# Kernel tuning notes

Hardware: AMD Instinct MI355X
Metric: run time of the kernel (lower is better)

The kernel has to match this reference:

```python
import jax, jax.numpy as jnp
import numpy as np

MARGIN = 0.3
BIG = 9999999.0


def setup_inputs() -> dict:
    key = jax.random.key(0)
    k1, k2, k3 = jax.random.split(key, 3)
    N, D, D2, NUM_IDS = 8192, 1024, 512, 512
    emb = jax.random.normal(k1, (N, D), dtype=jnp.float32)
    clot_feats_s = jax.random.normal(k2, (N, D2), dtype=jnp.float32)
    label = jax.random.randint(k3, (N,), 0, NUM_IDS, dtype=jnp.int64)
    return {"emb": emb, "label": label, "clot_feats_s": clot_feats_s}


def _margin_ranking_loss(x1, x2, y, margin):
    # torch MarginRankingLoss: mean(max(0, -y*(x1-x2)+margin))
    return jnp.mean(jnp.maximum(0.0, -y * (x1 - x2) + margin))


def reference(emb, label, clot_feats_s):
    N = emb.shape[0]
    # euclidean_dist(emb, emb): [N,N]
    sq = jnp.sum(emb * emb, axis=1)
    dist = sq[:, None] + sq[None, :] - 2.0 * (emb @ emb.T)
    dist = jnp.sqrt(jnp.clip(dist, 1e-12, None))
    # cosine similarity of clot_feats_s with itself: [N,N]
    nrm = jnp.sqrt(jnp.sum(clot_feats_s * clot_feats_s, axis=1))
    cos = (clot_feats_s @ clot_feats_s.T) / (nrm[:, None] * nrm[None, :])
    # same-identity mask
    sim = (label[:, None] == label[None, :]).astype(dist.dtype)
    # batch-hard: top-2 positives (largest masked distance), hardest negative (smallest)
    pos_vals, pos_idx = jax.lax.top_k(dist - BIG * (1.0 - sim), 2)
    dist_ap1, dist_ap2 = pos_vals[:, 0], pos_vals[:, 1]
    neg_mat = dist + BIG * sim
    hard_n_idx = jnp.argmin(neg_mat, axis=1)
    dist_an = jnp.min(neg_mat, axis=1)
    rows = jnp.arange(N)
    # per-row gathers into cosine-sim matrix (detached in original)
    alpha1 = jax.lax.stop_gradient(cos[rows, pos_idx[:, 0]])
    alpha2 = jax.lax.stop_gradient(cos[rows, pos_idx[:, 1]])
    # (alphan gathered in original but unused in the loss)
    y11 = jnp.where(alpha1 < alpha2, -1.0, 1.0)
    y11_m = jnp.where(alpha1 == alpha2, 0.0, 1.0)
    loss11 = _margin_ranking_loss(
        dist_ap2 * y11_m,
        dist_ap1 * y11_m + MARGIN * (alpha1 - alpha2 - y11),
        y11, MARGIN)
    dist_ap1_m = dist_ap1 + MARGIN * (alpha1 - 1.0)
    loss13 = _margin_ranking_loss(dist_an, dist_ap1_m, 1.0, MARGIN)
    loss = 0.1 * loss11 + loss13
    prec = jnp.mean((dist_an > dist_ap1_m).astype(jnp.float32))
    return loss, prec
```

## Files before the change

### kernel.cpp

```cpp
#include <hip/hip_runtime.h>
#include <stdint.h>

#define NR 8192
#define DE 1024
#define DC 512
#define BIGF 9999999.0f
#define MARG 0.3f
#define NEGI -3.0e38f
#define POSI 3.0e38f

typedef __attribute__((ext_vector_type(8))) short bf16x8;
typedef __attribute__((ext_vector_type(4))) float f32x4;

typedef __attribute__((address_space(3))) unsigned int lds_u32;
typedef const __attribute__((address_space(1))) unsigned int glb_u32;

static __device__ __forceinline__ void ld_g2l16(const void* g, void* l) {
    __builtin_amdgcn_global_load_lds((glb_u32*)g, (lds_u32*)l, 16, 0, 0);
}

static __device__ __forceinline__ unsigned short f2bf(float x) {
    unsigned u = __float_as_uint(x);
    unsigned r = u + 0x7FFFu + ((u >> 16) & 1u);
    return (unsigned short)(r >> 16);
}

static __device__ __forceinline__ float b2f(short u) {
    return __uint_as_float(((unsigned)(unsigned short)u) << 16);
}

__global__ __launch_bounds__(256) void k_prep_emb(const float* __restrict__ emb,
                                                  const int* __restrict__ label,
                                                  short* __restrict__ embb,
                                                  float* __restrict__ sq,
                                                  int* __restrict__ cnt) {
    int row = blockIdx.x, tid = threadIdx.x;
    float4 v = ((const float4*)(emb + (size_t)row * DE))[tid];
    float s = v.x * v.x + v.y * v.y + v.z * v.z + v.w * v.w;
    ushort4 b;
    b.x = f2bf(v.x); b.y = f2bf(v.y); b.z = f2bf(v.z); b.w = f2bf(v.w);
    *(ushort4*)&embb[(size_t)row * DE + tid * 4] = b;
    for (int m = 1; m < 64; m <<= 1) s += __shfl_xor(s, m);
    __shared__ float red[4];
    if ((tid & 63) == 0) red[tid >> 6] = s;
    __syncthreads();
    if (tid == 0) {
        sq[row] = red[0] + red[1] + red[2] + red[3];
        atomicAdd(&cnt[label[row]], 1);
    }
}

__global__ __launch_bounds__(256) void k_fill(const int* __restrict__ cnt,
                                              const int* __restrict__ label,
                                              int* __restrict__ clsOff,
                                              int* __restrict__ fill,
                                              int* __restrict__ list) {
    __shared__ int s[512];
    int t = threadIdx.x;
    s[t] = cnt[t];
    s[t + 256] = cnt[t + 256];
    __syncthreads();
    for (int d = 1; d < 512; d <<= 1) {
        int v0 = (t >= d) ? s[t - d] : 0;
        int v1 = s[t + 256 - d];
        __syncthreads();
        s[t] += v0;
        s[t + 256] += v1;
        __syncthreads();
    }
    if (blockIdx.x == 0) {
        clsOff[t] = s[t] - cnt[t];
        clsOff[t + 256] = s[t + 256] - cnt[t + 256];
    }
    int i = blockIdx.x * 256 + t;
    int l = label[i];
    int p = atomicAdd(&fill[l], 1);
    list[s[l] - cnt[l] + p] = i;
}

__global__ __launch_bounds__(256, 4) void k_main(const short* __restrict__ embb,
                                                 const float* __restrict__ sq,
                                                 const int* __restrict__ label,
                                                 unsigned* __restrict__ mnA) {
    const int b = blockIdx.x;
    int r = (int)((129.0f - sqrtf(16641.0f - 8.0f * (float)b)) * 0.5f);
    if (r < 0) r = 0;
    if (r > 63) r = 63;
    while (r > 0 && 64 * r - (r * (r - 1)) / 2 > b) --r;
    while (64 * (r + 1) - ((r + 1) * r) / 2 <= b) ++r;
    const int c = r + (b - (64 * r - (r * (r - 1)) / 2));
    const int i0 = r * 128, j0 = c * 128;

    __shared__ __align__(16) short As[128 * 32];
    __shared__ __align__(16) short Bs[128 * 32];

    const int tid = threadIdx.x;
    const int lane = tid & 63;
    const int w = tid >> 6;
    const int wr = w >> 1, wc = w & 1;
    const int q = lane >> 4, l15 = lane & 15;

    const int srow = tid >> 2;
    const int g = (tid & 3) ^ ((tid >> 3) & 3);
    const short* gA = embb + (size_t)(i0 + srow) * DE + g * 8;
    const short* gB = embb + (size_t)(j0 + srow) * DE + g * 8;

    const int pxor = q ^ ((l15 >> 1) & 3);

    auto stage = [&](int koff) {
        ld_g2l16(gA + koff, &As[(size_t)tid * 8]);
        ld_g2l16(gA + (size_t)64 * DE + koff, &As[(size_t)(tid + 256) * 8]);
        ld_g2l16(gB + koff, &Bs[(size_t)tid * 8]);
        ld_g2l16(gB + (size_t)64 * DE + koff, &Bs[(size_t)(tid + 256) * 8]);
    };

    stage(0);

    f32x4 acc[4][4];
#pragma unroll
    for (int mi = 0; mi < 4; ++mi)
#pragma unroll
        for (int ni = 0; ni < 4; ++ni) acc[mi][ni] = (f32x4){0.f, 0.f, 0.f, 0.f};

    for (int ks = 0; ks < 32; ++ks) {
        __syncthreads();
        bf16x8 af[4], bfr[4];
#pragma unroll
        for (int mi = 0; mi < 4; ++mi)
            af[mi] = *(const bf16x8*)&As[(wr * 64 + mi * 16 + l15) * 32 + pxor * 8];
#pragma unroll
        for (int ni = 0; ni < 4; ++ni)
            bfr[ni] = *(const bf16x8*)&Bs[(wc * 64 + ni * 16 + l15) * 32 + pxor * 8];
#pragma unroll
        for (int mi = 0; mi < 4; ++mi)
#pragma unroll
            for (int ni = 0; ni < 4; ++ni)
                acc[mi][ni] = __builtin_amdgcn_mfma_f32_16x16x32_bf16(af[mi], bfr[ni], acc[mi][ni], 0, 0, 0);
        __syncthreads();
        if (ks < 31) stage((ks + 1) * 32);
    }

    const int rb = i0 + wr * 64, cb = j0 + wc * 64;
    float sqj[4]; int lbj[4]; float cmn[4];
#pragma unroll
    for (int ni = 0; ni < 4; ++ni) {
        int cg = cb + ni * 16 + l15;
        sqj[ni] = sq[cg]; lbj[ni] = label[cg]; cmn[ni] = POSI;
    }
#pragma unroll
    for (int mi = 0; mi < 4; ++mi) {
        float rm[4] = {POSI, POSI, POSI, POSI};
        float sqi[4]; int lbi[4];
#pragma unroll
        for (int rr = 0; rr < 4; ++rr) {
            int rg = rb + mi * 16 + q * 4 + rr;
            sqi[rr] = sq[rg]; lbi[rr] = label[rg];
        }
#pragma unroll
        for (int ni = 0; ni < 4; ++ni)
#pragma unroll
            for (int rr = 0; rr < 4; ++rr) {
                float d2 = fmaf(-2.0f, acc[mi][ni][rr], sqi[rr] + sqj[ni]);
                d2 = fmaxf(d2, 1e-12f);
                float dn = (lbi[rr] == lbj[ni]) ? POSI : d2;
                rm[rr] = fminf(rm[rr], dn);
                cmn[ni] = fminf(cmn[ni], dn);
            }
#pragma unroll
        for (int rr = 0; rr < 4; ++rr) {
            float v = rm[rr];
            v = fminf(v, __shfl_xor(v, 1));
            v = fminf(v, __shfl_xor(v, 2));
            v = fminf(v, __shfl_xor(v, 4));
            v = fminf(v, __shfl_xor(v, 8));
            if (l15 == 0) atomicMin(&mnA[rb + mi * 16 + q * 4 + rr], __float_as_uint(v));
        }
    }
#pragma unroll
    for (int ni = 0; ni < 4; ++ni) {
        float v = cmn[ni];
        v = fminf(v, __shfl_xor(v, 16));
        v = fminf(v, __shfl_xor(v, 32));
        if (q == 0) atomicMin(&mnA[cb + ni * 16 + l15], __float_as_uint(v));
    }
}

__global__ __launch_bounds__(256) void k_pos(const short* __restrict__ embb,
                                             const float* __restrict__ sq,
                                             const float* __restrict__ clot,
                                             const int* __restrict__ label,
                                             const int* __restrict__ cnt,
                                             const int* __restrict__ clsOff,
                                             const int* __restrict__ clsList,
                                             const unsigned* __restrict__ mnA,
                                             float* __restrict__ ap1, float* __restrict__ ap2,
                                             float* __restrict__ an,
                                             float* __restrict__ alpha1, float* __restrict__ alpha2) {
    int wid = threadIdx.x >> 6, lane = threadIdx.x & 63;
    int row = blockIdx.x * 4 + wid;
    int lb = label[row];
    int cc = cnt[lb], off = clsOff[lb];
    float sqiv = sq[row];

    const bf16x8* rp = (const bf16x8*)(embb + (size_t)row * DE + lane * 16);
    bf16x8 ra = rp[0], rb = rp[1];
    float rf[16];
#pragma unroll
    for (int t = 0; t < 8; ++t) { rf[t] = b2f(ra[t]); rf[8 + t] = b2f(rb[t]); }

    float v1 = NEGI, v2 = NEGI;
    int i1 = 0, i2 = 0;
    for (int m = 0; m < cc; ++m) {
        int j = clsList[off + m];
        float d2;
        if (j == row) {
            d2 = 1e-12f;
        } else {
            const bf16x8* jp = (const bf16x8*)(embb + (size_t)j * DE + lane * 16);
            bf16x8 ja = jp[0], jb = jp[1];
            float s = 0.f;
#pragma unroll
            for (int t = 0; t < 8; ++t) s = fmaf(rf[t], b2f(ja[t]), s);
#pragma unroll
            for (int t = 0; t < 8; ++t) s = fmaf(rf[8 + t], b2f(jb[t]), s);
            for (int mm = 1; mm < 64; mm <<= 1) s += __shfl_xor(s, mm);
            d2 = fmaxf(fmaf(-2.0f, s, sqiv + sq[j]), 1e-12f);
        }
        bool t1 = (d2 > v1) || (d2 == v1 && j < i1);
        bool t2 = (d2 > v2) || (d2 == v2 && j < i2);
        v2 = t1 ? v1 : (t2 ? d2 : v2);
        i2 = t1 ? i1 : (t2 ? j : i2);
        v1 = t1 ? d2 : v1;
        i1 = t1 ? j : i1;
    }

    float a1 = sqrtf(v1);
    int j1 = i1;
    float a2v; int j2;
    if (cc >= 2) {
        a2v = sqrtf(v2);
        j2 = i2;
    } else {
        float kv = NEGI; int ki = 0;
        for (int c = lane; c < NR; c += 64) {
            if (label[c] == lb) continue;
            float s = 0.f;
            const short* crow = embb + (size_t)c * DE;
            const short* rrow = embb + (size_t)row * DE;
            for (int t = 0; t < DE; ++t) s = fmaf(b2f(rrow[t]), b2f(crow[t]), s);
            float d2c = fmaxf(fmaf(-2.0f, s, sqiv + sq[c]), 1e-12f);
            bool tk = (d2c > kv) || (d2c == kv && c < ki);
            kv = tk ? d2c : kv; ki = tk ? c : ki;
        }
        for (int mm = 1; mm < 64; mm <<= 1) {
            float ov = __shfl_xor(kv, mm); int oi = __shfl_xor(ki, mm);
            bool tk = (ov > kv) || (ov == kv && oi < ki);
            kv = tk ? ov : kv; ki = tk ? oi : ki;
        }
        a2v = sqrtf(kv) - BIGF;
        j2 = ki;
    }

    const float4* c4 = (const float4*)clot;
    float s1 = 0.f, s2 = 0.f, n0 = 0.f, n1 = 0.f, n2 = 0.f;
    for (int t = lane; t < DC / 4; t += 64) {
        float4 a = c4[(size_t)row * (DC / 4) + t];
        float4 b1 = c4[(size_t)j1 * (DC / 4) + t];
        float4 b2 = c4[(size_t)j2 * (DC / 4) + t];
        s1 += a.x * b1.x + a.y * b1.y + a.z * b1.z + a.w * b1.w;
        s2 += a.x * b2.x + a.y * b2.y + a.z * b2.z + a.w * b2.w;
        n0 += a.x * a.x + a.y * a.y + a.z * a.z + a.w * a.w;
        n1 += b1.x * b1.x + b1.y * b1.y + b1.z * b1.z + b1.w * b1.w;
        n2 += b2.x * b2.x + b2.y * b2.y + b2.z * b2.z + b2.w * b2.w;
    }
    for (int mm = 1; mm < 64; mm <<= 1) {
        s1 += __shfl_xor(s1, mm); s2 += __shfl_xor(s2, mm);
        n0 += __shfl_xor(n0, mm); n1 += __shfl_xor(n1, mm); n2 += __shfl_xor(n2, mm);
    }
    if (lane == 0) {
        ap1[row] = a1; ap2[row] = a2v;
        an[row] = sqrtf(__uint_as_float(mnA[row]));
        alpha1[row] = s1 / (sqrtf(n0) * sqrtf(n1));
        alpha2[row] = s2 / (sqrtf(n0) * sqrtf(n2));
    }
}

__global__ __launch_bounds__(256) void k_final(const float* __restrict__ ap1, const float* __restrict__ ap2,
                                               const float* __restrict__ an,
                                               const float* __restrict__ alpha1, const float* __restrict__ alpha2,
                                               float* __restrict__ out) {
    int tid = threadIdx.x;
    float sl11 = 0.f, sl13 = 0.f, sp = 0.f;
    for (int row = tid; row < NR; row += 256) {
        float a1 = alpha1[row], a2 = alpha2[row];
        float dap1 = ap1[row], dap2 = ap2[row], dan = an[row];
        float y = (a1 < a2) ? -1.f : 1.f;
        float ym = (a1 == a2) ? 0.f : 1.f;
        float x1 = dap2 * ym;
        float x2 = dap1 * ym + MARG * (a1 - a2 - y);
        sl11 += fmaxf(0.f, -y * (x1 - x2) + MARG);
        float ap1m = dap1 + MARG * (a1 - 1.f);
        sl13 += fmaxf(0.f, -(dan - ap1m) + MARG);
        sp += (dan > ap1m) ? 1.f : 0.f;
    }
    for (int m = 1; m < 64; m <<= 1) {
        sl11 += __shfl_xor(sl11, m);
        sl13 += __shfl_xor(sl13, m);
        sp += __shfl_xor(sp, m);
    }
    __shared__ float r11[4], r13[4], rp[4];
    if ((tid & 63) == 0) { r11[tid >> 6] = sl11; r13[tid >> 6] = sl13; rp[tid >> 6] = sp; }
    __syncthreads();
    if (tid == 0) {
        float t11 = r11[0] + r11[1] + r11[2] + r11[3];
        float t13 = r13[0] + r13[1] + r13[2] + r13[3];
        float tp = rp[0] + rp[1] + rp[2] + rp[3];
        out[0] = 0.1f * (t11 / (float)NR) + t13 / (float)NR;
        out[1] = tp / (float)NR;
    }
}

extern "C" void kernel_launch(void* const* d_in, const int* in_sizes, int n_in,
                              void* d_out, int out_size, void* d_ws, size_t ws_size,
                              hipStream_t stream) {
    const float* emb = (const float*)d_in[0];
    const int* label = (const int*)d_in[1];
    const float* clot = (const float*)d_in[2];
    float* out = (float*)d_out;

    char* ws = (char*)d_ws;
    size_t off = 0;
    auto alloc = [&](size_t bytes) -> char* {
        char* p = ws + off;
        off = (off + bytes + 255) & ~(size_t)255;
        return p;
    };
    short*    embb = (short*)alloc((size_t)NR * DE * 2);
    float*    sq   = (float*)alloc(NR * 4);
    int*      cnt  = (int*)alloc(512 * 4);
    int*      fill = (int*)alloc(512 * 4);
    int*      cOff = (int*)alloc(512 * 4);
    int*      list = (int*)alloc(NR * 4);
    unsigned* mnA  = (unsigned*)alloc((size_t)NR * 4);
    float*    ap1  = (float*)alloc(NR * 4);
    float*    ap2  = (float*)alloc(NR * 4);
    float*    an   = (float*)alloc(NR * 4);
    float*    al1  = (float*)alloc(NR * 4);
    float*    al2  = (float*)alloc(NR * 4);

    hipMemsetAsync(cnt, 0, 2 * 512 * 4, stream);
    hipMemsetAsync(mnA, 0xFF, (size_t)NR * 4, stream);

    k_prep_emb<<<dim3(NR), dim3(256), 0, stream>>>(emb, label, embb, sq, cnt);
    k_fill<<<dim3(NR / 256), dim3(256), 0, stream>>>(cnt, label, cOff, fill, list);
    k_main<<<dim3(2080), dim3(256), 0, stream>>>(embb, sq, label, mnA);
    k_pos<<<dim3(NR / 4), dim3(256), 0, stream>>>(embb, sq, clot, label, cnt, cOff, list,
                                                  mnA, ap1, ap2, an, al1, al2);
    k_final<<<dim3(1), dim3(256), 0, stream>>>(ap1, ap2, an, al1, al2, out);
}
```

Measured before the change: 247.5 us.

## Widen main GEMM tile to 128x256 with double-buffered LDS staging

```diff
diff --git a/kernel.cpp b/kernel.cpp
--- a/kernel.cpp
+++ b/kernel.cpp
@@ -78,21 +78,20 @@
     list[s[l] - cnt[l] + p] = i;
 }
 
-__global__ __launch_bounds__(256, 4) void k_main(const short* __restrict__ embb,
+__global__ __launch_bounds__(256, 2) void k_main(const short* __restrict__ embb,
                                                  const float* __restrict__ sq,
                                                  const int* __restrict__ label,
                                                  unsigned* __restrict__ mnA) {
     const int b = blockIdx.x;
-    int r = (int)((129.0f - sqrtf(16641.0f - 8.0f * (float)b)) * 0.5f);
-    if (r < 0) r = 0;
-    if (r > 63) r = 63;
-    while (r > 0 && 64 * r - (r * (r - 1)) / 2 > b) --r;
-    while (64 * (r + 1) - ((r + 1) * r) / 2 <= b) ++r;
-    const int c = r + (b - (64 * r - (r * (r - 1)) / 2));
-    const int i0 = r * 128, j0 = c * 128;
-
-    __shared__ __align__(16) short As[128 * 32];
-    __shared__ __align__(16) short Bs[128 * 32];
+    int c2 = (int)((sqrtf(1.0f + 4.0f * (float)b) - 1.0f) * 0.5f);
+    if (c2 < 0) c2 = 0;
+    while (c2 > 0 && c2 * c2 + c2 > b) --c2;
+    while ((c2 + 1) * (c2 + 1) + (c2 + 1) <= b) ++c2;
+    const int r = b - c2 * c2 - c2;
+    const int i0 = r * 128, j0 = c2 * 256;
+
+    __shared__ __align__(16) short As[2][128 * 32];
+    __shared__ __align__(16) short Bs[2][256 * 32];
 
     const int tid = threadIdx.x;
     const int lane = tid & 63;
@@ -107,43 +106,46 @@
 
     const int pxor = q ^ ((l15 >> 1) & 3);
 
-    auto stage = [&](int koff) {
-        ld_g2l16(gA + koff, &As[(size_t)tid * 8]);
-        ld_g2l16(gA + (size_t)64 * DE + koff, &As[(size_t)(tid + 256) * 8]);
-        ld_g2l16(gB + koff, &Bs[(size_t)tid * 8]);
-        ld_g2l16(gB + (size_t)64 * DE + koff, &Bs[(size_t)(tid + 256) * 8]);
+    auto stage = [&](int koff, int p) {
+        ld_g2l16(gA + koff, &As[p][(size_t)tid * 8]);
+        ld_g2l16(gA + (size_t)64 * DE + koff, &As[p][(size_t)(tid + 256) * 8]);
+        ld_g2l16(gB + koff, &Bs[p][(size_t)tid * 8]);
+        ld_g2l16(gB + (size_t)64 * DE + koff, &Bs[p][(size_t)(tid + 256) * 8]);
+        ld_g2l16(gB + (size_t)128 * DE + koff, &Bs[p][(size_t)(tid + 512) * 8]);
+        ld_g2l16(gB + (size_t)192 * DE + koff, &Bs[p][(size_t)(tid + 768) * 8]);
     };
 
-    stage(0);
-
-    f32x4 acc[4][4];
+    stage(0, 0);
+    int p = 0;
+
+    f32x4 acc[4][8];
 #pragma unroll
     for (int mi = 0; mi < 4; ++mi)
 #pragma unroll
-        for (int ni = 0; ni < 4; ++ni) acc[mi][ni] = (f32x4){0.f, 0.f, 0.f, 0.f};
+        for (int ni = 0; ni < 8; ++ni) acc[mi][ni] = (f32x4){0.f, 0.f, 0.f, 0.f};
 
     for (int ks = 0; ks < 32; ++ks) {
         __syncthreads();
-        bf16x8 af[4], bfr[4];
+        if (ks < 31) stage((ks + 1) * 32, p ^ 1);
+        bf16x8 af[4], bfr[8];
 #pragma unroll
         for (int mi = 0; mi < 4; ++mi)
-            af[mi] = *(const bf16x8*)&As[(wr * 64 + mi * 16 + l15) * 32 + pxor * 8];
-#pragma unroll
-        for (int ni = 0; ni < 4; ++ni)
-            bfr[ni] = *(const bf16x8*)&Bs[(wc * 64 + ni * 16 + l15) * 32 + pxor * 8];
+            af[mi] = *(const bf16x8*)&As[p][(wr * 64 + mi * 16 + l15) * 32 + pxor * 8];
+#pragma unroll
+        for (int ni = 0; ni < 8; ++ni)
+            bfr[ni] = *(const bf16x8*)&Bs[p][(wc * 128 + ni * 16 + l15) * 32 + pxor * 8];
 #pragma unroll
         for (int mi = 0; mi < 4; ++mi)
 #pragma unroll
-            for (int ni = 0; ni < 4; ++ni)
+            for (int ni = 0; ni < 8; ++ni)
                 acc[mi][ni] = __builtin_amdgcn_mfma_f32_16x16x32_bf16(af[mi], bfr[ni], acc[mi][ni], 0, 0, 0);
-        __syncthreads();
-        if (ks < 31) stage((ks + 1) * 32);
-    }
-
-    const int rb = i0 + wr * 64, cb = j0 + wc * 64;
-    float sqj[4]; int lbj[4]; float cmn[4];
-#pragma unroll
-    for (int ni = 0; ni < 4; ++ni) {
+        p ^= 1;
+    }
+
+    const int rb = i0 + wr * 64, cb = j0 + wc * 128;
+    float sqj[8]; int lbj[8]; float cmn[8];
+#pragma unroll
+    for (int ni = 0; ni < 8; ++ni) {
         int cg = cb + ni * 16 + l15;
         sqj[ni] = sq[cg]; lbj[ni] = label[cg]; cmn[ni] = POSI;
     }
@@ -157,7 +159,7 @@
             sqi[rr] = sq[rg]; lbi[rr] = label[rg];
         }
 #pragma unroll
-        for (int ni = 0; ni < 4; ++ni)
+        for (int ni = 0; ni < 8; ++ni)
 #pragma unroll
             for (int rr = 0; rr < 4; ++rr) {
                 float d2 = fmaf(-2.0f, acc[mi][ni][rr], sqi[rr] + sqj[ni]);
@@ -177,7 +179,7 @@
         }
     }
 #pragma unroll
-    for (int ni = 0; ni < 4; ++ni) {
+    for (int ni = 0; ni < 8; ++ni) {
         float v = cmn[ni];
         v = fminf(v, __shfl_xor(v, 16));
         v = fminf(v, __shfl_xor(v, 32));
@@ -353,7 +355,7 @@
 
     k_prep_emb<<<dim3(NR), dim3(256), 0, stream>>>(emb, label, embb, sq, cnt);
     k_fill<<<dim3(NR / 256), dim3(256), 0, stream>>>(cnt, label, cOff, fill, list);
-    k_main<<<dim3(2080), dim3(256), 0, stream>>>(embb, sq, label, mnA);
+    k_main<<<dim3(1056), dim3(256), 0, stream>>>(embb, sq, label, mnA);
     k_pos<<<dim3(NR / 4), dim3(256), 0, stream>>>(embb, sq, clot, label, cnt, cOff, list,
                                                   mnA, ap1, ap2, an, al1, al2);
     k_final<<<dim3(1), dim3(256), 0, stream>>>(ap1, ap2, an, al1, al2, out);
```

Result: slower. 253.8 us (+2.5%).

## Double GEMM K-tile to 64 with wider swizzle and unroll positive-pair loop

Applied to the files above, without the earlier changes.

```diff
diff --git a/kernel.cpp b/kernel.cpp
--- a/kernel.cpp
+++ b/kernel.cpp
@@ -78,7 +78,7 @@
     list[s[l] - cnt[l] + p] = i;
 }
 
-__global__ __launch_bounds__(256, 4) void k_main(const short* __restrict__ embb,
+__global__ __launch_bounds__(256, 3) void k_main(const short* __restrict__ embb,
                                                  const float* __restrict__ sq,
                                                  const int* __restrict__ label,
                                                  unsigned* __restrict__ mnA) {
@@ -91,8 +91,8 @@
     const int c = r + (b - (64 * r - (r * (r - 1)) / 2));
     const int i0 = r * 128, j0 = c * 128;
 
-    __shared__ __align__(16) short As[128 * 32];
-    __shared__ __align__(16) short Bs[128 * 32];
+    __shared__ __align__(16) short As[128 * 64];
+    __shared__ __align__(16) short Bs[128 * 64];
 
     const int tid = threadIdx.x;
     const int lane = tid & 63;
@@ -100,18 +100,18 @@
     const int wr = w >> 1, wc = w & 1;
     const int q = lane >> 4, l15 = lane & 15;
 
-    const int srow = tid >> 2;
-    const int g = (tid & 3) ^ ((tid >> 3) & 3);
-    const short* gA = embb + (size_t)(i0 + srow) * DE + g * 8;
-    const short* gB = embb + (size_t)(j0 + srow) * DE + g * 8;
-
-    const int pxor = q ^ ((l15 >> 1) & 3);
+    const int g = (tid & 7) ^ ((tid >> 3) & 7);
+    const short* gA = embb + (size_t)(i0 + (tid >> 3)) * DE + g * 8;
+    const short* gB = embb + (size_t)(j0 + (tid >> 3)) * DE + g * 8;
+
+    const int swz = l15 & 7;
 
     auto stage = [&](int koff) {
-        ld_g2l16(gA + koff, &As[(size_t)tid * 8]);
-        ld_g2l16(gA + (size_t)64 * DE + koff, &As[(size_t)(tid + 256) * 8]);
-        ld_g2l16(gB + koff, &Bs[(size_t)tid * 8]);
-        ld_g2l16(gB + (size_t)64 * DE + koff, &Bs[(size_t)(tid + 256) * 8]);
+#pragma unroll
+        for (int n = 0; n < 4; ++n) {
+            ld_g2l16(gA + (size_t)n * 32 * DE + koff, &As[n * 2048 + tid * 8]);
+            ld_g2l16(gB + (size_t)n * 32 * DE + koff, &Bs[n * 2048 + tid * 8]);
+        }
     };
 
     stage(0);
@@ -122,22 +122,28 @@
 #pragma unroll
         for (int ni = 0; ni < 4; ++ni) acc[mi][ni] = (f32x4){0.f, 0.f, 0.f, 0.f};
 
-    for (int ks = 0; ks < 32; ++ks) {
+    for (int ks = 0; ks < 16; ++ks) {
         __syncthreads();
-        bf16x8 af[4], bfr[4];
-#pragma unroll
-        for (int mi = 0; mi < 4; ++mi)
-            af[mi] = *(const bf16x8*)&As[(wr * 64 + mi * 16 + l15) * 32 + pxor * 8];
-#pragma unroll
-        for (int ni = 0; ni < 4; ++ni)
-            bfr[ni] = *(const bf16x8*)&Bs[(wc * 64 + ni * 16 + l15) * 32 + pxor * 8];
-#pragma unroll
-        for (int mi = 0; mi < 4; ++mi)
+        bf16x8 af[2][4], bfr[2][4];
+#pragma unroll
+        for (int kk = 0; kk < 2; ++kk) {
+            const int kc = ((kk * 4 + q) ^ swz) * 8;
+#pragma unroll
+            for (int mi = 0; mi < 4; ++mi)
+                af[kk][mi] = *(const bf16x8*)&As[(wr * 64 + mi * 16 + l15) * 64 + kc];
 #pragma unroll
             for (int ni = 0; ni < 4; ++ni)
-                acc[mi][ni] = __builtin_amdgcn_mfma_f32_16x16x32_bf16(af[mi], bfr[ni], acc[mi][ni], 0, 0, 0);
+                bfr[kk][ni] = *(const bf16x8*)&Bs[(wc * 64 + ni * 16 + l15) * 64 + kc];
+        }
+#pragma unroll
+        for (int kk = 0; kk < 2; ++kk)
+#pragma unroll
+            for (int mi = 0; mi < 4; ++mi)
+#pragma unroll
+                for (int ni = 0; ni < 4; ++ni)
+                    acc[mi][ni] = __builtin_amdgcn_mfma_f32_16x16x32_bf16(af[kk][mi], bfr[kk][ni], acc[mi][ni], 0, 0, 0);
         __syncthreads();
-        if (ks < 31) stage((ks + 1) * 32);
+        if (ks < 15) stage((ks + 1) * 64);
     }
 
     const int rb = i0 + wr * 64, cb = j0 + wc * 64;
@@ -210,28 +216,53 @@
 
     float v1 = NEGI, v2 = NEGI;
     int i1 = 0, i2 = 0;
-    for (int m = 0; m < cc; ++m) {
+
+    auto upd = [&](float d2, int j) {
+        bool t1 = (d2 > v1) || (d2 == v1 && j < i1);
+        bool t2 = (d2 > v2) || (d2 == v2 && j < i2);
+        v2 = t1 ? v1 : (t2 ? d2 : v2);
+        i2 = t1 ? i1 : (t2 ? j : i2);
+        v1 = t1 ? d2 : v1;
+        i1 = t1 ? j : i1;
+    };
+
+    int m = 0;
+    for (; m + 2 <= cc; m += 2) {
+        int ja = clsList[off + m], jb = clsList[off + m + 1];
+        const bf16x8* pa = (const bf16x8*)(embb + (size_t)ja * DE + lane * 16);
+        const bf16x8* pb = (const bf16x8*)(embb + (size_t)jb * DE + lane * 16);
+        bf16x8 a0 = pa[0], a1v = pa[1];
+        bf16x8 b0 = pb[0], b1v = pb[1];
+        float sa = 0.f, sb = 0.f;
+#pragma unroll
+        for (int t = 0; t < 8; ++t) { sa = fmaf(rf[t], b2f(a0[t]), sa); sb = fmaf(rf[t], b2f(b0[t]), sb); }
+#pragma unroll
+        for (int t = 0; t < 8; ++t) { sa = fmaf(rf[8 + t], b2f(a1v[t]), sa); sb = fmaf(rf[8 + t], b2f(b1v[t]), sb); }
+        for (int mm = 1; mm < 64; mm <<= 1) { sa += __shfl_xor(sa, mm); sb += __shfl_xor(sb, mm); }
+        float d2a = fmaxf(fmaf(-2.0f, sa, sqiv + sq[ja]), 1e-12f);
+        float d2b = fmaxf(fmaf(-2.0f, sb, sqiv + sq[jb]), 1e-12f);
+        if (ja == row) d2a = 1e-12f;
+        if (jb == row) d2b = 1e-12f;
+        upd(d2a, ja);
+        upd(d2b, jb);
+    }
+    if (m < cc) {
         int j = clsList[off + m];
         float d2;
         if (j == row) {
             d2 = 1e-12f;
         } else {
             const bf16x8* jp = (const bf16x8*)(embb + (size_t)j * DE + lane * 16);
-            bf16x8 ja = jp[0], jb = jp[1];
+            bf16x8 ja0 = jp[0], ja1 = jp[1];
             float s = 0.f;
 #pragma unroll
-            for (int t = 0; t < 8; ++t) s = fmaf(rf[t], b2f(ja[t]), s);
-#pragma unroll
-            for (int t = 0; t < 8; ++t) s = fmaf(rf[8 + t], b2f(jb[t]), s);
+            for (int t = 0; t < 8; ++t) s = fmaf(rf[t], b2f(ja0[t]), s);
+#pragma unroll
+            for (int t = 0; t < 8; ++t) s = fmaf(rf[8 + t], b2f(ja1[t]), s);
             for (int mm = 1; mm < 64; mm <<= 1) s += __shfl_xor(s, mm);
             d2 = fmaxf(fmaf(-2.0f, s, sqiv + sq[j]), 1e-12f);
         }
-        bool t1 = (d2 > v1) || (d2 == v1 && j < i1);
-        bool t2 = (d2 > v2) || (d2 == v2 && j < i2);
-        v2 = t1 ? v1 : (t2 ? d2 : v2);
-        i2 = t1 ? i1 : (t2 ? j : i2);
-        v1 = t1 ? d2 : v1;
-        i1 = t1 ? j : i1;
+        upd(d2, j);
     }
 
     float a1 = sqrtf(v1);
@@ -242,15 +273,15 @@
         j2 = i2;
     } else {
         float kv = NEGI; int ki = 0;
-        for (int c = lane; c < NR; c += 64) {
-            if (label[c] == lb) continue;
+        for (int cr = lane; cr < NR; cr += 64) {
+            if (label[cr] == lb) continue;
             float s = 0.f;
-            const short* crow = embb + (size_t)c * DE;
+            const short* crow = embb + (size_t)cr * DE;
             const short* rrow = embb + (size_t)row * DE;
             for (int t = 0; t < DE; ++t) s = fmaf(b2f(rrow[t]), b2f(crow[t]), s);
-            float d2c = fmaxf(fmaf(-2.0f, s, sqiv + sq[c]), 1e-12f);
-            bool tk = (d2c > kv) || (d2c == kv && c < ki);
-            kv = tk ? d2c : kv; ki = tk ? c : ki;
+            float d2c = fmaxf(fmaf(-2.0f, s, sqiv + sq[cr]), 1e-12f);
+            bool tk = (d2c > kv) || (d2c == kv && cr < ki);
+            kv = tk ? d2c : kv; ki = tk ? cr : ki;
         }
         for (int mm = 1; mm < 64; mm <<= 1) {
             float ov = __shfl_xor(kv, mm); int oi = __shfl_xor(ki, mm);
```

Result: faster. 232.7 us (-6.0%).
